# Optimization experiments

Hardware: AMD Instinct MI355X
Metric: run time of the kernel (lower is better)

The kernel has to match this reference:

```python
import jax, jax.numpy as jnp
import numpy as np

SQRT_QKV_DIM = 8.0  # sqrt(qkv_dim=64)


def setup_inputs() -> dict:
    key = jax.random.key(0)
    ks = jax.random.split(key, 8)
    B, H, T, M, d, hid = 4, 16, 512, 512, 64, 16
    return {
        "q": jax.random.normal(ks[0], (B, H, T, d), dtype=jnp.float32),
        "k": jax.random.normal(ks[1], (B, H, M, d), dtype=jnp.float32),
        "v": jax.random.normal(ks[2], (B, H, M, d), dtype=jnp.float32),
        "D_TM": jax.random.uniform(ks[3], (B, T, M), dtype=jnp.float32),
        "mix1_weight": jax.random.uniform(ks[4], (H, 2, hid), minval=-0.7071, maxval=0.7071, dtype=jnp.float32),
        "mix1_bias": jax.random.uniform(ks[5], (H, hid), minval=-0.7071, maxval=0.7071, dtype=jnp.float32),
        "mix2_weight": jax.random.uniform(ks[6], (H, hid, 1), minval=-0.25, maxval=0.25, dtype=jnp.float32),
        "mix2_bias": jax.random.uniform(ks[7], (H, 1), minval=-0.25, maxval=0.25, dtype=jnp.float32),
    }


def reference(q, k, v, D_TM, mix1_weight, mix1_bias, mix2_weight, mix2_bias):
    B, H, T, d = q.shape
    Mc = k.shape[2]
    # scaled dot-product score: (B,H,T,M)
    dot_score = jnp.einsum("bhtd,bhmd->bhtm", q, k) / SQRT_QKV_DIM
    # per-head 2->hidden->1 MLP mixing dot score and distance bias.
    # Avoid explicit stack: linear layer over the 2 score channels expands as
    # dot*W1[:,0,:] + D*W1[:,1,:].  ms1: (B,H,T,M,hid)
    w1_dot = mix1_weight[:, 0, :][None, :, None, None, :]   # (1,H,1,1,hid)
    w1_dist = mix1_weight[:, 1, :][None, :, None, None, :]
    ms1 = (dot_score[..., None] * w1_dot
           + D_TM[:, None, :, :, None] * w1_dist
           + mix1_bias[None, :, None, None, :])
    ms1 = jax.nn.relu(ms1)
    # hidden -> 1: mixed_scores (B,H,T,M)
    mixed = jnp.einsum("bhtmc,hc->bhtm", ms1, mix2_weight[:, :, 0])
    mixed = mixed + mix2_bias[:, 0][None, :, None, None]
    weights = jax.nn.softmax(mixed, axis=3)
    out = jnp.einsum("bhtm,bhmd->bhtd", weights, v)   # (B,H,T,d)
    return out.transpose(0, 2, 1, 3).reshape(B, T, H * d)
```

## Files before the change

### kernel.cpp

```cpp
#include <hip/hip_runtime.h>
#include <stdint.h>

typedef __attribute__((ext_vector_type(8))) short short8;
typedef __attribute__((ext_vector_type(4))) float floatx4;

#define MFMA(a, b, c) __builtin_amdgcn_mfma_f32_16x16x32_bf16(a, b, c, 0, 0, 0)

union Frag { uint32_t u[4]; short8 s; };

__device__ __forceinline__ void packsplit(float a, float b, uint32_t& hi, uint32_t& lo) {
    uint32_t ua = __float_as_uint(a), ub = __float_as_uint(b);
    uint32_t ha = ua & 0xFFFF0000u, hb = ub & 0xFFFF0000u;
    float ra = a - __uint_as_float(ha);
    float rb = b - __uint_as_float(hb);
    hi = (ha >> 16) | hb;
    lo = (__float_as_uint(ra) >> 16) | (__float_as_uint(rb) & 0xFFFF0000u);
}

#define KHI 0
#define KLO 4608
#define VTHI 0
#define VTLO 4352
#define PHI 8704
#define PLO 13056

__global__ __launch_bounds__(256, 2)
void msmha_mfma(const float* __restrict__ qg, const float* __restrict__ kg,
                const float* __restrict__ vg, const float* __restrict__ Dg,
                const float* __restrict__ m1w, const float* __restrict__ m1b,
                const float* __restrict__ m2w, const float* __restrict__ m2b,
                float* __restrict__ outg) {
    __shared__ __align__(16) uint32_t sm[17408];
    __shared__ __align__(16) float wlds[68];

    const int tid  = threadIdx.x;
    const int w    = tid >> 6;
    const int lane = tid & 63;
    const int col  = lane & 15;
    const int quad = lane >> 4;

    const int bid = blockIdx.x;
    const int wgT = bid & 7;
    const int bh  = bid >> 3;
    const int h   = bh & 15;
    const int b   = bh >> 4;
    const int t0g = wgT * 64;

    const size_t base = (size_t)bh * 512 * 64;

    if (tid < 16) {
        wlds[4 * tid + 0] = m1w[h * 32 + tid];
        wlds[4 * tid + 1] = m1w[h * 32 + 16 + tid];
        wlds[4 * tid + 2] = m1b[h * 16 + tid];
        wlds[4 * tid + 3] = m2w[h * 16 + tid];
    }
    if (tid == 16) wlds[64] = m2b[h];

    Frag qh[2], ql[2];
    {
        const float* qrow = qg + base + (size_t)(t0g + w * 16 + col) * 64;
#pragma unroll
        for (int ks = 0; ks < 2; ++ks) {
            const float4 f0 = *(const float4*)(qrow + ks * 32 + quad * 8);
            const float4 f1 = *(const float4*)(qrow + ks * 32 + quad * 8 + 4);
            packsplit(f0.x, f0.y, qh[ks].u[0], ql[ks].u[0]);
            packsplit(f0.z, f0.w, qh[ks].u[1], ql[ks].u[1]);
            packsplit(f1.x, f1.y, qh[ks].u[2], ql[ks].u[2]);
            packsplit(f1.z, f1.w, qh[ks].u[3], ql[ks].u[3]);
        }
    }

    floatx4 accA[32];

    const float* Dbase = Dg + ((size_t)b * 512 + t0g + w * 16 + col) * 512 + quad * 4;

#pragma unroll
    for (int mc = 0; mc < 4; ++mc) {
        __syncthreads();
#pragma unroll
        for (int it = 0; it < 8; ++it) {
            const int i  = tid + it * 256;
            const int ml = i >> 4, k4 = i & 15;
            const float4 f = *(const float4*)(kg + base + (size_t)(mc * 128 + ml) * 64 + k4 * 4);
            uint32_t h0, l0, h1, l1;
            packsplit(f.x, f.y, h0, l0);
            packsplit(f.z, f.w, h1, l1);
            *(uint2*)(sm + KHI + ml * 36 + 2 * k4) = make_uint2(h0, h1);
            *(uint2*)(sm + KLO + ml * 36 + 2 * k4) = make_uint2(l0, l1);
        }
        __syncthreads();

        float4 dv[8];
#pragma unroll
        for (int mt = 0; mt < 8; ++mt)
            dv[mt] = *(const float4*)(Dbase + mc * 128 + mt * 16);

#pragma unroll
        for (int mt = 0; mt < 8; ++mt) {
            floatx4 acc = {0.f, 0.f, 0.f, 0.f};
#pragma unroll
            for (int ks = 0; ks < 2; ++ks) {
                const int ro = (mt * 16 + col) * 36 + 16 * ks + 4 * quad;
                Frag ah, al;
                ah.s = *(short8*)(sm + KHI + ro);
                al.s = *(short8*)(sm + KLO + ro);
                acc = MFMA(ah.s, qh[ks].s, acc);
                acc = MFMA(ah.s, ql[ks].s, acc);
                acc = MFMA(al.s, qh[ks].s, acc);
            }
            accA[mc * 8 + mt] = acc;
        }

        float mix[32];
        const float b2v = wlds[64];
#pragma unroll
        for (int mt = 0; mt < 8; ++mt)
#pragma unroll
            for (int r = 0; r < 4; ++r) {
                accA[mc * 8 + mt][r] *= 0.125f;
                mix[mt * 4 + r] = b2v;
            }
#pragma unroll 1
        for (int c = 0; c < 16; ++c) {
            const float4 wv = *(const float4*)(wlds + 4 * c);
#pragma unroll
            for (int mt = 0; mt < 8; ++mt) {
                const float4 dd = dv[mt];
                const float dr[4] = {dd.x, dd.y, dd.z, dd.w};
#pragma unroll
                for (int r = 0; r < 4; ++r) {
                    const float hh = fmaf(accA[mc * 8 + mt][r], wv.x, fmaf(dr[r], wv.y, wv.z));
                    mix[mt * 4 + r] = fmaf(fmaxf(hh, 0.f), wv.w, mix[mt * 4 + r]);
                }
            }
        }
#pragma unroll
        for (int mt = 0; mt < 8; ++mt)
#pragma unroll
            for (int r = 0; r < 4; ++r)
                accA[mc * 8 + mt][r] = mix[mt * 4 + r];
    }

    float mx = -3.4e38f;
#pragma unroll
    for (int i = 0; i < 32; ++i)
#pragma unroll
        for (int r = 0; r < 4; ++r) mx = fmaxf(mx, accA[i][r]);
    mx = fmaxf(mx, __shfl_xor(mx, 16, 64));
    mx = fmaxf(mx, __shfl_xor(mx, 32, 64));
    float sum = 0.f;
#pragma unroll
    for (int i = 0; i < 32; ++i)
#pragma unroll
        for (int r = 0; r < 4; ++r) {
            const float e = __expf(accA[i][r] - mx);
            accA[i][r] = e;
            sum += e;
        }
    sum += __shfl_xor(sum, 16, 64);
    sum += __shfl_xor(sum, 32, 64);
    const float rinv = 1.f / sum;
#pragma unroll
    for (int i = 0; i < 32; ++i)
#pragma unroll
        for (int r = 0; r < 4; ++r) accA[i][r] *= rinv;

    floatx4 oacc[4];
#pragma unroll
    for (int dt = 0; dt < 4; ++dt) oacc[dt] = floatx4{0.f, 0.f, 0.f, 0.f};

#pragma unroll
    for (int mc = 0; mc < 4; ++mc) {
        __syncthreads();
#pragma unroll
        for (int it = 0; it < 4; ++it) {
            const int u  = tid + it * 256;
            const int d4 = u & 15, m2 = u >> 4;
            const float4 f0 = *(const float4*)(vg + base + (size_t)(mc * 128 + 2 * m2) * 64 + d4 * 4);
            const float4 f1 = *(const float4*)(vg + base + (size_t)(mc * 128 + 2 * m2 + 1) * 64 + d4 * 4);
            const float a0[4] = {f0.x, f0.y, f0.z, f0.w};
            const float a1[4] = {f1.x, f1.y, f1.z, f1.w};
#pragma unroll
            for (int i = 0; i < 4; ++i) {
                uint32_t hw, lw;
                packsplit(a0[i], a1[i], hw, lw);
                sm[VTHI + (d4 * 4 + i) * 68 + m2] = hw;
                sm[VTLO + (d4 * 4 + i) * 68 + m2] = lw;
            }
        }
        {
            const int prow = (w * 16 + col) * 68;
#pragma unroll
            for (int mt = 0; mt < 8; ++mt) {
                const floatx4 pv = accA[mc * 8 + mt];
                uint32_t h0, l0, h1, l1;
                packsplit(pv[0], pv[1], h0, l0);
                packsplit(pv[2], pv[3], h1, l1);
                *(uint2*)(sm + PHI + prow + mt * 8 + 2 * quad) = make_uint2(h0, h1);
                *(uint2*)(sm + PLO + prow + mt * 8 + 2 * quad) = make_uint2(l0, l1);
            }
        }
        __syncthreads();
#pragma unroll
        for (int ks = 0; ks < 4; ++ks) {
            const int po = (w * 16 + col) * 68 + 16 * ks + 4 * quad;
            Frag pah, pal;
            pah.s = *(short8*)(sm + PHI + po);
            pal.s = *(short8*)(sm + PLO + po);
#pragma unroll
            for (int dt = 0; dt < 4; ++dt) {
                const int vo = (dt * 16 + col) * 68 + 16 * ks + 4 * quad;
                Frag bh, bl;
                bh.s = *(short8*)(sm + VTHI + vo);
                bl.s = *(short8*)(sm + VTLO + vo);
                oacc[dt] = MFMA(pah.s, bh.s, oacc[dt]);
                oacc[dt] = MFMA(pah.s, bl.s, oacc[dt]);
                oacc[dt] = MFMA(pal.s, bh.s, oacc[dt]);
            }
        }
    }

    const size_t obase = ((size_t)b * 512 + t0g + w * 16 + quad * 4) * 1024 + h * 64 + col;
#pragma unroll
    for (int dt = 0; dt < 4; ++dt)
#pragma unroll
        for (int r = 0; r < 4; ++r)
            outg[obase + (size_t)r * 1024 + dt * 16] = oacc[dt][r];
}

extern "C" void kernel_launch(void* const* d_in, const int* in_sizes, int n_in,
                              void* d_out, int out_size, void* d_ws, size_t ws_size,
                              hipStream_t stream) {
    const float* q   = (const float*)d_in[0];
    const float* k   = (const float*)d_in[1];
    const float* v   = (const float*)d_in[2];
    const float* dtm = (const float*)d_in[3];
    const float* m1w = (const float*)d_in[4];
    const float* m1b = (const float*)d_in[5];
    const float* m2w = (const float*)d_in[6];
    const float* m2b = (const float*)d_in[7];
    float* out = (float*)d_out;

    dim3 grid(4 * 16 * 8);
    dim3 block(256);
    msmha_mfma<<<grid, block, 0, stream>>>(q, k, v, dtm, m1w, m1b, m2w, m2b, out);
}
```

Measured before the change: 133.8 us.

## Rewrite relu-MLP via abs identity, double-buffer K/V tiles, defer softmax normalization

Replaces relu(h)*w2 with 0.5*w2*|h| plus a linear term folded into precomputed per-head constants, with log2e folded in so the softmax can use exp2. K and V staging becomes 64-row double-buffered tiles, prefetched into registers while the current tile is computed, so there is one barrier per chunk. V is stored with a rotated layout to reduce LDS bank conflicts, and softmax normalization is moved to the output store. The changes cut VALU work in the mixing loop and hide global load latency, at the cost of more registers and each thread redundantly computing the per-head constants.

New measurement: 134.5 us. About the same (+0.5%).

```diff
diff --git a/kernel.cpp b/kernel.cpp
--- a/kernel.cpp
+++ b/kernel.cpp
@@ -17,12 +17,16 @@
     lo = (__float_as_uint(ra) >> 16) | (__float_as_uint(rb) & 0xFFFF0000u);
 }
 
-#define KHI 0
-#define KLO 4608
-#define VTHI 0
-#define VTLO 4352
-#define PHI 8704
-#define PLO 13056
+__device__ __forceinline__ float fexp2(float x) {
+#if __has_builtin(__builtin_amdgcn_exp2f)
+    return __builtin_amdgcn_exp2f(x);
+#else
+    return exp2f(x);
+#endif
+}
+
+#define PHIo 9216
+#define PLOo 11520
 
 __global__ __launch_bounds__(256, 2)
 void msmha_mfma(const float* __restrict__ qg, const float* __restrict__ kg,
@@ -30,8 +34,8 @@
                 const float* __restrict__ m1w, const float* __restrict__ m1b,
                 const float* __restrict__ m2w, const float* __restrict__ m2b,
                 float* __restrict__ outg) {
-    __shared__ __align__(16) uint32_t sm[17408];
-    __shared__ __align__(16) float wlds[68];
+    __shared__ __align__(16) uint32_t sm[13824];
+    __shared__ __align__(16) float4 wlds[16];
 
     const int tid  = threadIdx.x;
     const int w    = tid >> 6;
@@ -47,14 +51,27 @@
     const int t0g = wgT * 64;
 
     const size_t base = (size_t)bh * 512 * 64;
+    const float LOG2E = 1.4426950408889634f;
 
     if (tid < 16) {
-        wlds[4 * tid + 0] = m1w[h * 32 + tid];
-        wlds[4 * tid + 1] = m1w[h * 32 + 16 + tid];
-        wlds[4 * tid + 2] = m1b[h * 16 + tid];
-        wlds[4 * tid + 3] = m2w[h * 16 + tid];
-    }
-    if (tid == 16) wlds[64] = m2b[h];
+        const float w1d = m1w[h * 32 + tid];
+        const float w1s = m1w[h * 32 + 16 + tid];
+        const float b1  = m1b[h * 16 + tid];
+        const float w2  = m2w[h * 16 + tid];
+        wlds[tid] = make_float4(w1d * (0.125f * LOG2E), w1s * LOG2E, b1 * LOG2E, 0.5f * w2);
+    }
+
+    float sA = 0.f, sB = 0.f, sC = 0.f;
+#pragma unroll 1
+    for (int c = 0; c < 16; ++c) {
+        const float w2 = m2w[h * 16 + c];
+        sA = fmaf(w2, m1w[h * 32 + c], sA);
+        sB = fmaf(w2, m1w[h * 32 + 16 + c], sB);
+        sC = fmaf(w2, m1b[h * 16 + c], sC);
+    }
+    const float Ac = sA * (0.0625f * LOG2E);
+    const float Bc = sB * (0.5f * LOG2E);
+    const float Cc = fmaf(0.5f, sC, m2b[h]) * LOG2E;
 
     Frag qh[2], ql[2];
     {
@@ -71,75 +88,121 @@
     }
 
     floatx4 accA[32];
-
     const float* Dbase = Dg + ((size_t)b * 512 + t0g + w * 16 + col) * 512 + quad * 4;
 
-#pragma unroll
-    for (int mc = 0; mc < 4; ++mc) {
-        __syncthreads();
-#pragma unroll
-        for (int it = 0; it < 8; ++it) {
-            const int i  = tid + it * 256;
-            const int ml = i >> 4, k4 = i & 15;
-            const float4 f = *(const float4*)(kg + base + (size_t)(mc * 128 + ml) * 64 + k4 * 4);
+    const int ml0 = tid >> 4;
+    const int k4  = tid & 15;
+    float4 kreg[4];
+    auto kload = [&](int mc) {
+#pragma unroll
+        for (int it = 0; it < 4; ++it)
+            kreg[it] = *(const float4*)(kg + base + (size_t)(mc * 64 + ml0 + it * 16) * 64 + k4 * 4);
+    };
+    auto kwrite = [&](int p) {
+        uint32_t* KH = sm + p * 4608;
+        uint32_t* KL = KH + 2304;
+#pragma unroll
+        for (int it = 0; it < 4; ++it) {
             uint32_t h0, l0, h1, l1;
-            packsplit(f.x, f.y, h0, l0);
-            packsplit(f.z, f.w, h1, l1);
-            *(uint2*)(sm + KHI + ml * 36 + 2 * k4) = make_uint2(h0, h1);
-            *(uint2*)(sm + KLO + ml * 36 + 2 * k4) = make_uint2(l0, l1);
-        }
-        __syncthreads();
-
-        float4 dv[8];
-#pragma unroll
-        for (int mt = 0; mt < 8; ++mt)
-            dv[mt] = *(const float4*)(Dbase + mc * 128 + mt * 16);
-
-#pragma unroll
-        for (int mt = 0; mt < 8; ++mt) {
+            packsplit(kreg[it].x, kreg[it].y, h0, l0);
+            packsplit(kreg[it].z, kreg[it].w, h1, l1);
+            const int ml = ml0 + it * 16;
+            *(uint2*)(KH + ml * 36 + 2 * k4) = make_uint2(h0, h1);
+            *(uint2*)(KL + ml * 36 + 2 * k4) = make_uint2(l0, l1);
+        }
+    };
+
+    kload(0);
+    kwrite(0);
+    __syncthreads();
+
+#pragma unroll
+    for (int mc = 0; mc < 8; ++mc) {
+        const int p = mc & 1;
+        if (mc < 7) kload(mc + 1);
+
+        float4 dv[4];
+#pragma unroll
+        for (int mt = 0; mt < 4; ++mt)
+            dv[mt] = *(const float4*)(Dbase + mc * 64 + mt * 16);
+
+        const uint32_t* KH = sm + p * 4608;
+        const uint32_t* KL = KH + 2304;
+        floatx4 sc[4];
+#pragma unroll
+        for (int mt = 0; mt < 4; ++mt) {
             floatx4 acc = {0.f, 0.f, 0.f, 0.f};
 #pragma unroll
             for (int ks = 0; ks < 2; ++ks) {
                 const int ro = (mt * 16 + col) * 36 + 16 * ks + 4 * quad;
                 Frag ah, al;
-                ah.s = *(short8*)(sm + KHI + ro);
-                al.s = *(short8*)(sm + KLO + ro);
+                ah.s = *(const short8*)(KH + ro);
+                al.s = *(const short8*)(KL + ro);
                 acc = MFMA(ah.s, qh[ks].s, acc);
                 acc = MFMA(ah.s, ql[ks].s, acc);
                 acc = MFMA(al.s, qh[ks].s, acc);
             }
-            accA[mc * 8 + mt] = acc;
-        }
-
-        float mix[32];
-        const float b2v = wlds[64];
-#pragma unroll
-        for (int mt = 0; mt < 8; ++mt)
-#pragma unroll
-            for (int r = 0; r < 4; ++r) {
-                accA[mc * 8 + mt][r] *= 0.125f;
-                mix[mt * 4 + r] = b2v;
-            }
-#pragma unroll 1
+            sc[mt] = acc;
+        }
+
+        float dvf[16];
+#pragma unroll
+        for (int mt = 0; mt < 4; ++mt) {
+            dvf[mt * 4 + 0] = dv[mt].x; dvf[mt * 4 + 1] = dv[mt].y;
+            dvf[mt * 4 + 2] = dv[mt].z; dvf[mt * 4 + 3] = dv[mt].w;
+        }
+        float mix[16];
+#pragma unroll
+        for (int e = 0; e < 16; ++e) mix[e] = fmaf(dvf[e], Bc, Cc);
+#pragma unroll 4
         for (int c = 0; c < 16; ++c) {
-            const float4 wv = *(const float4*)(wlds + 4 * c);
-#pragma unroll
-            for (int mt = 0; mt < 8; ++mt) {
-                const float4 dd = dv[mt];
-                const float dr[4] = {dd.x, dd.y, dd.z, dd.w};
+            const float4 wv = wlds[c];
+#pragma unroll
+            for (int mt = 0; mt < 4; ++mt)
 #pragma unroll
                 for (int r = 0; r < 4; ++r) {
-                    const float hh = fmaf(accA[mc * 8 + mt][r], wv.x, fmaf(dr[r], wv.y, wv.z));
-                    mix[mt * 4 + r] = fmaf(fmaxf(hh, 0.f), wv.w, mix[mt * 4 + r]);
+                    const float hh = fmaf(sc[mt][r], wv.x, fmaf(dvf[mt * 4 + r], wv.y, wv.z));
+                    mix[mt * 4 + r] = fmaf(fabsf(hh), wv.w, mix[mt * 4 + r]);
                 }
-            }
-        }
-#pragma unroll
-        for (int mt = 0; mt < 8; ++mt)
+        }
+#pragma unroll
+        for (int mt = 0; mt < 4; ++mt)
 #pragma unroll
             for (int r = 0; r < 4; ++r)
-                accA[mc * 8 + mt][r] = mix[mt * 4 + r];
-    }
+                accA[mc * 4 + mt][r] = fmaf(sc[mt][r], Ac, mix[mt * 4 + r]);
+
+        if (mc < 7) kwrite(p ^ 1);
+        __syncthreads();
+    }
+
+    const int dgrp = tid & 15, m4 = tid >> 4;
+    const int rotV = 8 * (dgrp & 3);
+    float4 vreg[4];
+    auto vload = [&](int mc) {
+#pragma unroll
+        for (int i = 0; i < 4; ++i)
+            vreg[i] = *(const float4*)(vg + base + (size_t)(mc * 64 + 4 * m4 + i) * 64 + dgrp * 4);
+    };
+    auto vwrite = [&](int p) {
+        uint32_t* VH = sm + p * 4608;
+        uint32_t* VL = VH + 2304;
+        const float a0[4] = {vreg[0].x, vreg[0].y, vreg[0].z, vreg[0].w};
+        const float a1[4] = {vreg[1].x, vreg[1].y, vreg[1].z, vreg[1].w};
+        const float a2[4] = {vreg[2].x, vreg[2].y, vreg[2].z, vreg[2].w};
+        const float a3[4] = {vreg[3].x, vreg[3].y, vreg[3].z, vreg[3].w};
+        const int cp = (2 * m4 + rotV) & 31;
+#pragma unroll
+        for (int jj = 0; jj < 4; ++jj) {
+            uint32_t h0, l0, h1, l1;
+            packsplit(a0[jj], a1[jj], h0, l0);
+            packsplit(a2[jj], a3[jj], h1, l1);
+            const int d = 4 * dgrp + jj;
+            *(uint2*)(VH + d * 36 + cp) = make_uint2(h0, h1);
+            *(uint2*)(VL + d * 36 + cp) = make_uint2(l0, l1);
+        }
+    };
+
+    vload(0);
 
     float mx = -3.4e38f;
 #pragma unroll
@@ -153,71 +216,66 @@
     for (int i = 0; i < 32; ++i)
 #pragma unroll
         for (int r = 0; r < 4; ++r) {
-            const float e = __expf(accA[i][r] - mx);
+            const float e = fexp2(accA[i][r] - mx);
             accA[i][r] = e;
             sum += e;
         }
     sum += __shfl_xor(sum, 16, 64);
     sum += __shfl_xor(sum, 32, 64);
-    const float rinv = 1.f / sum;
-#pragma unroll
-    for (int i = 0; i < 32; ++i)
-#pragma unroll
-        for (int r = 0; r < 4; ++r) accA[i][r] *= rinv;
+    const float rv = 1.f / sum;
+    float rinvT[4];
+#pragma unroll
+    for (int r = 0; r < 4; ++r)
+        rinvT[r] = __shfl(rv, quad * 4 + r, 64);
+
+    vwrite(0);
+    __syncthreads();
 
     floatx4 oacc[4];
 #pragma unroll
     for (int dt = 0; dt < 4; ++dt) oacc[dt] = floatx4{0.f, 0.f, 0.f, 0.f};
 
-#pragma unroll
-    for (int mc = 0; mc < 4; ++mc) {
-        __syncthreads();
-#pragma unroll
-        for (int it = 0; it < 4; ++it) {
-            const int u  = tid + it * 256;
-            const int d4 = u & 15, m2 = u >> 4;
-            const float4 f0 = *(const float4*)(vg + base + (size_t)(mc * 128 + 2 * m2) * 64 + d4 * 4);
-            const float4 f1 = *(const float4*)(vg + base + (size_t)(mc * 128 + 2 * m2 + 1) * 64 + d4 * 4);
-            const float a0[4] = {f0.x, f0.y, f0.z, f0.w};
-            const float a1[4] = {f1.x, f1.y, f1.z, f1.w};
-#pragma unroll
-            for (int i = 0; i < 4; ++i) {
-                uint32_t hw, lw;
-                packsplit(a0[i], a1[i], hw, lw);
-                sm[VTHI + (d4 * 4 + i) * 68 + m2] = hw;
-                sm[VTLO + (d4 * 4 + i) * 68 + m2] = lw;
-            }
-        }
-        {
-            const int prow = (w * 16 + col) * 68;
-#pragma unroll
-            for (int mt = 0; mt < 8; ++mt) {
-                const floatx4 pv = accA[mc * 8 + mt];
-                uint32_t h0, l0, h1, l1;
-                packsplit(pv[0], pv[1], h0, l0);
-                packsplit(pv[2], pv[3], h1, l1);
-                *(uint2*)(sm + PHI + prow + mt * 8 + 2 * quad) = make_uint2(h0, h1);
-                *(uint2*)(sm + PLO + prow + mt * 8 + 2 * quad) = make_uint2(l0, l1);
-            }
-        }
-        __syncthreads();
-#pragma unroll
-        for (int ks = 0; ks < 4; ++ks) {
-            const int po = (w * 16 + col) * 68 + 16 * ks + 4 * quad;
+    const int prow = (w * 16 + col) * 36;
+    const int rotR = 8 * (col >> 2);
+
+#pragma unroll
+    for (int mc = 0; mc < 8; ++mc) {
+        const int p = mc & 1;
+        if (mc < 7) vload(mc + 1);
+
+#pragma unroll
+        for (int mt = 0; mt < 4; ++mt) {
+            const floatx4 pv = accA[mc * 4 + mt];
+            uint32_t h0, l0, h1, l1;
+            packsplit(pv[0], pv[1], h0, l0);
+            packsplit(pv[2], pv[3], h1, l1);
+            *(uint2*)(sm + PHIo + prow + mt * 8 + 2 * quad) = make_uint2(h0, h1);
+            *(uint2*)(sm + PLOo + prow + mt * 8 + 2 * quad) = make_uint2(l0, l1);
+        }
+
+        const uint32_t* VH = sm + p * 4608;
+        const uint32_t* VL = VH + 2304;
+#pragma unroll
+        for (int ks = 0; ks < 2; ++ks) {
+            const int po = prow + 16 * ks + 4 * quad;
             Frag pah, pal;
-            pah.s = *(short8*)(sm + PHI + po);
-            pal.s = *(short8*)(sm + PLO + po);
+            pah.s = *(const short8*)(sm + PHIo + po);
+            pal.s = *(const short8*)(sm + PLOo + po);
+            const int cb = ((16 * ks + 4 * quad) + rotR) & 31;
 #pragma unroll
             for (int dt = 0; dt < 4; ++dt) {
-                const int vo = (dt * 16 + col) * 68 + 16 * ks + 4 * quad;
+                const int vo = (dt * 16 + col) * 36 + cb;
                 Frag bh, bl;
-                bh.s = *(short8*)(sm + VTHI + vo);
-                bl.s = *(short8*)(sm + VTLO + vo);
+                bh.s = *(const short8*)(VH + vo);
+                bl.s = *(const short8*)(VL + vo);
                 oacc[dt] = MFMA(pah.s, bh.s, oacc[dt]);
                 oacc[dt] = MFMA(pah.s, bl.s, oacc[dt]);
                 oacc[dt] = MFMA(pal.s, bh.s, oacc[dt]);
             }
         }
+
+        if (mc < 7) vwrite(p ^ 1);
+        __syncthreads();
     }
 
     const size_t obase = ((size_t)b * 512 + t0g + w * 16 + quad * 4) * 1024 + h * 64 + col;
@@ -225,7 +283,7 @@
     for (int dt = 0; dt < 4; ++dt)
 #pragma unroll
         for (int r = 0; r < 4; ++r)
-            outg[obase + (size_t)r * 1024 + dt * 16] = oacc[dt][r];
+            outg[obase + (size_t)r * 1024 + dt * 16] = oacc[dt][r] * rinvT[r];
 }
 
 extern "C" void kernel_launch(void* const* d_in, const int* in_sizes, int n_in,
```
